# Kernel tuning notes

Hardware: AMD Instinct MI355X
Metric: run time of the kernel (lower is better)

Reference implementation:

```python
import jax, jax.numpy as jnp
import numpy as np

B, N, C = 8, 4096, 512
H = 8
HD = C // H  # 64
SCALE = HD ** -0.5


def setup_inputs() -> dict:
    key = jax.random.key(0)
    ks = jax.random.split(key, 6)
    x = jax.random.normal(ks[0], (B, N, C), dtype=jnp.float32)
    # nn.Linear(dim, dim*3, bias=False): weight [3C, C]
    w_qkv = jax.random.normal(ks[1], (3 * C, C), dtype=jnp.float32) * (C ** -0.5)
    # nn.Linear(dim, dim): weight [C, C], bias [C]
    w_proj = jax.random.normal(ks[2], (C, C), dtype=jnp.float32) * (C ** -0.5)
    b_proj = jnp.zeros((C,), dtype=jnp.float32)
    w_q = jax.random.normal(ks[3], (H, HD), dtype=jnp.float32)
    w_k = jax.random.normal(ks[4], (H, HD), dtype=jnp.float32)
    return {"x": x, "w_qkv": w_qkv, "w_proj": w_proj, "b_proj": b_proj,
            "w_q": w_q, "w_k": w_k}


def reference(x, w_qkv, w_proj, b_proj, w_q, w_k):
    b, n, c = x.shape
    # qkv projection: [B,N,3C] -> (3, B, H, N, HD)
    qkv = jnp.einsum('bnc,dc->bnd', x, w_qkv)
    qkv = qkv.reshape(b, n, 3, H, HD).transpose(2, 0, 3, 1, 4)
    q, k, v = qkv[0], qkv[1], qkv[2]  # each [B,H,N,HD]

    # alpha attention pooling of q -> global query [B,H,HD]
    alpha = jax.nn.softmax(jnp.einsum('bhnc,hc->bhn', q, w_q) * SCALE, axis=-1)
    global_q = jnp.einsum('bhn,bhnc->bhc', alpha, q)

    # p = broadcast global_q over k; beta pooling of k -> global key
    p = global_q[:, :, None, :] * k  # [B,H,N,HD] (attn_drop is identity in eval)
    beta = jax.nn.softmax(jnp.einsum('bhnc,hc->bhn', p, w_k) * SCALE, axis=-1)
    global_k = jnp.einsum('bhn,bhnc->bhc', beta, k)

    # u = global_k broadcast * v, then merge heads
    u = global_k[:, :, None, :] * v  # [B,H,N,HD]
    u_flat = u.transpose(0, 2, 1, 3).reshape(b, n, c)
    q_flat = q.transpose(0, 2, 1, 3).reshape(b, n, c)

    out = jnp.einsum('bnc,dc->bnd', u_flat, w_proj) + b_proj + q_flat
    return out
```

## Files before the change

### kernel.cpp

```cpp
#include <hip/hip_runtime.h>
#include <hip/hip_bf16.h>
#include <math.h>

#define B_  8
#define N_  4096
#define C_  512
#define H_  8
#define HD_ 64
#define M_  (B_*N_)
#define K_  C_
#define D3_ (3*C_)
#define SCALE_ 0.125f
#define CH_ 8
#define CHN (N_/CH_)

using f32x4  = __attribute__((ext_vector_type(4))) float;
using bf16x8 = __attribute__((ext_vector_type(8))) short;

__device__ __forceinline__ unsigned short f2bf(float f) {
    unsigned int u = __builtin_bit_cast(unsigned int, f);
    u += 0x7FFFu + ((u >> 16) & 1u);
    return (unsigned short)(u >> 16);
}
__device__ __forceinline__ float bf2f(unsigned short s) {
    unsigned int u = ((unsigned int)s) << 16;
    return __builtin_bit_cast(float, u);
}

__device__ __forceinline__ void gl_lds16(const void* g, void* l) {
    __builtin_amdgcn_global_load_lds(
        (const __attribute__((address_space(1))) unsigned int*)(g),
        (__attribute__((address_space(3))) unsigned int*)(l), 16, 0, 0);
}

__global__ __launch_bounds__(256, 2)
void k_gemm1(const unsigned short* __restrict__ Ag, const unsigned short* __restrict__ Bg,
             float* __restrict__ outQ, unsigned short* __restrict__ outK,
             unsigned short* __restrict__ outV)
{
    __shared__ __align__(16) unsigned char lds[16384];
    const int m0 = blockIdx.x * 128;
    const int d0 = blockIdx.y * 128;
    const int t = threadIdx.x, lane = t & 63, w = t >> 6;
    const int wr = w >> 1, wc = w & 1;
    const int lrow = lane >> 2, lslot = lane & 3;
    const int fr = lane & 15, g = lane >> 4;

    f32x4 acc[4][4];
    #pragma unroll
    for (int i = 0; i < 4; ++i)
        #pragma unroll
        for (int j = 0; j < 4; ++j) acc[i][j] = (f32x4){0.f,0.f,0.f,0.f};

    for (int k0 = 0; k0 < K_; k0 += 32) {
        #pragma unroll
        for (int s = 0; s < 2; ++s) {
            const int seg = w*2 + s;
            const int row = seg*16 + lrow;
            const int ch  = lslot ^ ((row >> 1) & 3);
            gl_lds16(Ag + (size_t)(m0+row)*K_ + k0 + ch*8, lds + seg*1024);
            gl_lds16(Bg + (size_t)(d0+row)*K_ + k0 + ch*8, lds + 8192 + seg*1024);
        }
        __syncthreads();
        bf16x8 aF[4], bF[4];
        #pragma unroll
        for (int i = 0; i < 4; ++i) {
            const int r = wr*64 + i*16 + fr;
            const int sl = g ^ ((r >> 1) & 3);
            aF[i] = *(const bf16x8*)(lds + r*64 + sl*16);
        }
        #pragma unroll
        for (int j = 0; j < 4; ++j) {
            const int r = wc*64 + j*16 + fr;
            const int sl = g ^ ((r >> 1) & 3);
            bF[j] = *(const bf16x8*)(lds + 8192 + r*64 + sl*16);
        }
        #pragma unroll
        for (int i = 0; i < 4; ++i)
            #pragma unroll
            for (int j = 0; j < 4; ++j)
                acc[i][j] = __builtin_amdgcn_mfma_f32_16x16x32_bf16(aF[i], bF[j], acc[i][j], 0, 0, 0);
        __syncthreads();
    }

    #pragma unroll
    for (int i = 0; i < 4; ++i)
        #pragma unroll
        for (int j = 0; j < 4; ++j) {
            const int trow = wr*64 + i*16 + (lane >> 4)*4;
            const int tcol = wc*64 + j*16 + (lane & 15);
            const int d = d0 + tcol;
            #pragma unroll
            for (int p = 0; p < 4; ++p) {
                const size_t m = (size_t)(m0 + trow + p);
                const float vv = acc[i][j][p];
                if (d0 < C_)          outQ[m*C_ + d] = vv;
                else if (d0 < 2*C_)   outK[m*C_ + (d - C_)] = f2bf(vv);
                else                  outV[m*C_ + (d - 2*C_)] = f2bf(vv);
            }
        }
}

__global__ __launch_bounds__(256, 2)
void k_gemm2(const unsigned short* __restrict__ Ag, const unsigned short* __restrict__ Wpb,
             const float* __restrict__ bproj, float* __restrict__ out)
{
    __shared__ __align__(16) unsigned char lds[16384];
    const int m0 = blockIdx.x * 128;
    const int d0 = blockIdx.y * 128;
    const int b  = m0 >> 12;
    const unsigned short* Bg = Wpb + (size_t)b * C_ * C_;
    const int t = threadIdx.x, lane = t & 63, w = t >> 6;
    const int wr = w >> 1, wc = w & 1;
    const int lrow = lane >> 2, lslot = lane & 3;
    const int fr = lane & 15, g = lane >> 4;

    f32x4 acc[4][4];
    #pragma unroll
    for (int i = 0; i < 4; ++i)
        #pragma unroll
        for (int j = 0; j < 4; ++j) acc[i][j] = (f32x4){0.f,0.f,0.f,0.f};

    for (int k0 = 0; k0 < K_; k0 += 32) {
        #pragma unroll
        for (int s = 0; s < 2; ++s) {
            const int seg = w*2 + s;
            const int row = seg*16 + lrow;
            const int ch  = lslot ^ ((row >> 1) & 3);
            gl_lds16(Ag + (size_t)(m0+row)*K_ + k0 + ch*8, lds + seg*1024);
            gl_lds16(Bg + (size_t)(d0+row)*K_ + k0 + ch*8, lds + 8192 + seg*1024);
        }
        __syncthreads();
        bf16x8 aF[4], bF[4];
        #pragma unroll
        for (int i = 0; i < 4; ++i) {
            const int r = wr*64 + i*16 + fr;
            const int sl = g ^ ((r >> 1) & 3);
            aF[i] = *(const bf16x8*)(lds + r*64 + sl*16);
        }
        #pragma unroll
        for (int j = 0; j < 4; ++j) {
            const int r = wc*64 + j*16 + fr;
            const int sl = g ^ ((r >> 1) & 3);
            bF[j] = *(const bf16x8*)(lds + 8192 + r*64 + sl*16);
        }
        #pragma unroll
        for (int i = 0; i < 4; ++i)
            #pragma unroll
            for (int j = 0; j < 4; ++j)
                acc[i][j] = __builtin_amdgcn_mfma_f32_16x16x32_bf16(aF[i], bF[j], acc[i][j], 0, 0, 0);
        __syncthreads();
    }

    #pragma unroll
    for (int i = 0; i < 4; ++i)
        #pragma unroll
        for (int j = 0; j < 4; ++j) {
            const int trow = wr*64 + i*16 + (lane >> 4)*4;
            const int tcol = wc*64 + j*16 + (lane & 15);
            const int d = d0 + tcol;
            const float bp = bproj[d];
            #pragma unroll
            for (int p = 0; p < 4; ++p) {
                const size_t off = (size_t)(m0 + trow + p)*C_ + d;
                out[off] = acc[i][j][p] + bp + out[off];
            }
        }
}

template<int SRCBF>
__device__ __forceinline__ float loadsrc(const void* s, size_t idx) {
    if constexpr (SRCBF) return bf2f(((const unsigned short*)s)[idx]);
    else                 return ((const float*)s)[idx];
}

template<int SRCBF>
__global__ __launch_bounds__(256)
void k_pool_part(const void* __restrict__ srcv, const float* __restrict__ wvec,
                 const float* __restrict__ gq_in,
                 float* __restrict__ pm, float* __restrict__ ps, float* __restrict__ pv)
{
    __shared__ float sl[CHN];
    __shared__ float red[4];
    __shared__ float stat[2];
    __shared__ float wsum[4][64];
    const int bid = blockIdx.x;
    const int bh = bid >> 3, ch = bid & 7;
    const int b = bh >> 3, h = bh & 7;
    const int t = threadIdx.x, lane = t & 63, wv = t >> 6;

    float w = wvec[h*HD_ + lane];
    if (gq_in) w *= gq_in[bh*HD_ + lane];
    const size_t rowbase = ((size_t)b*N_ + (size_t)ch*CHN)*C_ + h*HD_ + lane;

    for (int n0 = wv*4; n0 < CHN; n0 += 16) {
        float x0 = loadsrc<SRCBF>(srcv, rowbase + (size_t)(n0+0)*C_) * w;
        float x1 = loadsrc<SRCBF>(srcv, rowbase + (size_t)(n0+1)*C_) * w;
        float x2 = loadsrc<SRCBF>(srcv, rowbase + (size_t)(n0+2)*C_) * w;
        float x3 = loadsrc<SRCBF>(srcv, rowbase + (size_t)(n0+3)*C_) * w;
        #pragma unroll
        for (int off = 32; off; off >>= 1) {
            x0 += __shfl_xor(x0, off); x1 += __shfl_xor(x1, off);
            x2 += __shfl_xor(x2, off); x3 += __shfl_xor(x3, off);
        }
        if (lane == 0) {
            sl[n0+0] = x0*SCALE_; sl[n0+1] = x1*SCALE_;
            sl[n0+2] = x2*SCALE_; sl[n0+3] = x3*SCALE_;
        }
    }
    __syncthreads();

    float m = fmaxf(sl[t], sl[t+256]);
    #pragma unroll
    for (int off = 32; off; off >>= 1) m = fmaxf(m, __shfl_xor(m, off));
    if (lane == 0) red[wv] = m;
    __syncthreads();
    if (t == 0) stat[0] = fmaxf(fmaxf(red[0], red[1]), fmaxf(red[2], red[3]));
    __syncthreads();
    m = stat[0];

    float e0 = __expf(sl[t] - m), e1 = __expf(sl[t+256] - m);
    sl[t] = e0; sl[t+256] = e1;
    float s = e0 + e1;
    #pragma unroll
    for (int off = 32; off; off >>= 1) s += __shfl_xor(s, off);
    if (lane == 0) red[wv] = s;
    __syncthreads();
    if (t == 0) stat[1] = red[0] + red[1] + red[2] + red[3];
    __syncthreads();

    float acc = 0.f;
    for (int n0 = wv*4; n0 < CHN; n0 += 16) {
        acc = fmaf(sl[n0+0], loadsrc<SRCBF>(srcv, rowbase + (size_t)(n0+0)*C_), acc);
        acc = fmaf(sl[n0+1], loadsrc<SRCBF>(srcv, rowbase + (size_t)(n0+1)*C_), acc);
        acc = fmaf(sl[n0+2], loadsrc<SRCBF>(srcv, rowbase + (size_t)(n0+2)*C_), acc);
        acc = fmaf(sl[n0+3], loadsrc<SRCBF>(srcv, rowbase + (size_t)(n0+3)*C_), acc);
    }
    wsum[wv][lane] = acc;
    __syncthreads();
    if (t < 64) {
        pv[(size_t)bid*HD_ + t] = wsum[0][t] + wsum[1][t] + wsum[2][t] + wsum[3][t];
        if (t == 0) { pm[bid] = stat[0]; ps[bid] = stat[1]; }
    }
}

__global__ __launch_bounds__(64)
void k_pool_comb(const float* __restrict__ pm, const float* __restrict__ ps,
                 const float* __restrict__ pv, float* __restrict__ gout)
{
    const int bh = blockIdx.x, c = threadIdx.x;
    float m = -1e30f;
    #pragma unroll
    for (int ch = 0; ch < CH_; ++ch) m = fmaxf(m, pm[bh*CH_ + ch]);
    float s = 0.f, g = 0.f;
    #pragma unroll
    for (int ch = 0; ch < CH_; ++ch) {
        const float e = __expf(pm[bh*CH_ + ch] - m);
        s += ps[bh*CH_ + ch] * e;
        g += pv[(size_t)(bh*CH_ + ch)*HD_ + c] * e;
    }
    gout[bh*HD_ + c] = g / s;
}

__global__ void k_cvt(const float* __restrict__ in, unsigned short* __restrict__ o, int n4)
{
    int i = blockIdx.x*blockDim.x + threadIdx.x;
    const int stride = gridDim.x*blockDim.x;
    for (; i < n4; i += stride) {
        const float4 f = ((const float4*)in)[i];
        ushort4 r; r.x = f2bf(f.x); r.y = f2bf(f.y); r.z = f2bf(f.z); r.w = f2bf(f.w);
        ((ushort4*)o)[i] = r;
    }
}

__global__ void k_fold(const float* __restrict__ wp, const float* __restrict__ gkf,
                       unsigned short* __restrict__ wpb)
{
    const int i = blockIdx.x*256 + threadIdx.x;
    const int idx4 = i*4;
    const int b  = idx4 >> 18;
    const int wi = idx4 & 262143;
    const int k  = idx4 & 511;
    const float4 wv4 = *(const float4*)(wp + wi);
    const float* gk = gkf + b*C_ + k;
    ushort4 r;
    r.x = f2bf(wv4.x * gk[0]); r.y = f2bf(wv4.y * gk[1]);
    r.z = f2bf(wv4.z * gk[2]); r.w = f2bf(wv4.w * gk[3]);
    ((ushort4*)wpb)[i] = r;
}

extern "C" void kernel_launch(void* const* d_in, const int* in_sizes, int n_in,
                              void* d_out, int out_size, void* d_ws, size_t ws_size,
                              hipStream_t stream)
{
    (void)in_sizes; (void)n_in; (void)out_size; (void)ws_size;
    const float* x      = (const float*)d_in[0];
    const float* w_qkv  = (const float*)d_in[1];
    const float* w_proj = (const float*)d_in[2];
    const float* b_proj = (const float*)d_in[3];
    const float* w_q    = (const float*)d_in[4];
    const float* w_k    = (const float*)d_in[5];
    float* out = (float*)d_out;

    unsigned short* xb  = (unsigned short*)d_ws;
    unsigned short* wqb = xb  + (size_t)M_*K_;
    unsigned short* kb  = wqb + (size_t)D3_*K_;
    unsigned short* vb  = kb  + (size_t)M_*C_;
    unsigned short* wpb = vb  + (size_t)M_*C_;
    float* gq  = (float*)(wpb + (size_t)8*C_*C_);
    float* gkf = gq  + B_*H_*HD_;
    float* pm  = gkf + B_*H_*HD_;
    float* ps  = pm + 64*CH_;
    float* pv  = ps + 64*CH_;

    k_cvt<<<2048, 256, 0, stream>>>(x, xb, M_*K_/4);
    k_cvt<<<768,  256, 0, stream>>>(w_qkv, wqb, D3_*K_/4);

    dim3 g1(M_/128, D3_/128);
    k_gemm1<<<g1, 256, 0, stream>>>(xb, wqb, out, kb, vb);

    k_pool_part<0><<<64*CH_, 256, 0, stream>>>(out, w_q, nullptr, pm, ps, pv);
    k_pool_comb<<<64, 64, 0, stream>>>(pm, ps, pv, gq);
    k_pool_part<1><<<64*CH_, 256, 0, stream>>>(kb, w_k, gq, pm, ps, pv);
    k_pool_comb<<<64, 64, 0, stream>>>(pm, ps, pv, gkf);

    k_fold<<<2048, 256, 0, stream>>>(w_proj, gkf, wpb);

    dim3 g2(M_/128, C_/128);
    k_gemm2<<<g2, 256, 0, stream>>>(vb, wpb, b_proj, out);
}
```

Before: 308.6 us.

## Fuse alpha pooling into QKV GEMM epilogue and merge pooling stages

The q-side alpha softmax pooling now runs in the GEMM1 epilogue on the accumulators, writing per-16-row partial max/sum/weighted-vector results, so the separate pass that re-reads fp32 q from global memory goes away. The k-side pooling becomes a single-pass online softmax with 16 chunks per head, and the final combine is folded into the weight-fold kernel. The two conversion launches are merged into one. Launch count and memory traffic drop, at the cost of a heavier GEMM1 epilogue with shuffles and exps, plus a larger partial buffer (256 chunks per head) that comb1 must reduce.

```diff
diff --git a/kernel.cpp b/kernel.cpp
--- a/kernel.cpp
+++ b/kernel.cpp
@@ -11,8 +11,6 @@
 #define K_  C_
 #define D3_ (3*C_)
 #define SCALE_ 0.125f
-#define CH_ 8
-#define CHN (N_/CH_)
 
 using f32x4  = __attribute__((ext_vector_type(4))) float;
 using bf16x8 = __attribute__((ext_vector_type(8))) short;
@@ -35,8 +33,10 @@
 
 __global__ __launch_bounds__(256, 2)
 void k_gemm1(const unsigned short* __restrict__ Ag, const unsigned short* __restrict__ Bg,
+             const float* __restrict__ Wq,
              float* __restrict__ outQ, unsigned short* __restrict__ outK,
-             unsigned short* __restrict__ outV)
+             unsigned short* __restrict__ outV,
+             float* __restrict__ pm1, float* __restrict__ ps1, float* __restrict__ pv1)
 {
     __shared__ __align__(16) unsigned char lds[16384];
     const int m0 = blockIdx.x * 128;
@@ -87,8 +87,8 @@
     for (int i = 0; i < 4; ++i)
         #pragma unroll
         for (int j = 0; j < 4; ++j) {
-            const int trow = wr*64 + i*16 + (lane >> 4)*4;
-            const int tcol = wc*64 + j*16 + (lane & 15);
+            const int trow = wr*64 + i*16 + g*4;
+            const int tcol = wc*64 + j*16 + fr;
             const int d = d0 + tcol;
             #pragma unroll
             for (int p = 0; p < 4; ++p) {
@@ -99,6 +99,171 @@
                 else                  outV[m*C_ + (d - 2*C_)] = f2bf(vv);
             }
         }
+
+    if (d0 < C_) {
+        const int head = (d0 >> 6) + wc;
+        const int b = m0 >> 12;
+        const int bh = b*8 + head;
+        const int mchunk = (m0 & 4095) >> 7;
+        const int chunk = mchunk*8 + wr*4 + g;
+        float wqv[4];
+        #pragma unroll
+        for (int j = 0; j < 4; ++j) wqv[j] = Wq[head*HD_ + j*16 + fr] * SCALE_;
+
+        float s[4][4];
+        #pragma unroll
+        for (int i = 0; i < 4; ++i)
+            #pragma unroll
+            for (int p = 0; p < 4; ++p) {
+                float d = acc[i][0][p]*wqv[0] + acc[i][1][p]*wqv[1]
+                        + acc[i][2][p]*wqv[2] + acc[i][3][p]*wqv[3];
+                d += __shfl_xor(d, 1); d += __shfl_xor(d, 2);
+                d += __shfl_xor(d, 4); d += __shfl_xor(d, 8);
+                s[i][p] = d;
+            }
+        float mx = s[0][0];
+        #pragma unroll
+        for (int i = 0; i < 4; ++i)
+            #pragma unroll
+            for (int p = 0; p < 4; ++p) mx = fmaxf(mx, s[i][p]);
+        float e[4][4]; float ssum = 0.f;
+        #pragma unroll
+        for (int i = 0; i < 4; ++i)
+            #pragma unroll
+            for (int p = 0; p < 4; ++p) { e[i][p] = __expf(s[i][p] - mx); ssum += e[i][p]; }
+        #pragma unroll
+        for (int j = 0; j < 4; ++j) {
+            float pvj = 0.f;
+            #pragma unroll
+            for (int i = 0; i < 4; ++i)
+                #pragma unroll
+                for (int p = 0; p < 4; ++p) pvj = fmaf(e[i][p], acc[i][j][p], pvj);
+            pv1[((size_t)bh*256 + chunk)*64 + j*16 + fr] = pvj;
+        }
+        if (fr == 0) { pm1[bh*256 + chunk] = mx; ps1[bh*256 + chunk] = ssum; }
+    }
+}
+
+__global__ __launch_bounds__(256)
+void k_comb1(const float* __restrict__ pm, const float* __restrict__ ps,
+             const float* __restrict__ pv, float* __restrict__ gq)
+{
+    __shared__ float red[4];
+    __shared__ float sred[4];
+    __shared__ float pvs[4][64];
+    __shared__ float stat[2];
+    const int bh = blockIdx.x;
+    const int t = threadIdx.x, lane = t & 63, wv = t >> 6;
+
+    float m = pm[bh*256 + t];
+    #pragma unroll
+    for (int off = 32; off; off >>= 1) m = fmaxf(m, __shfl_xor(m, off));
+    if (lane == 0) red[wv] = m;
+    __syncthreads();
+    if (t == 0) stat[0] = fmaxf(fmaxf(red[0],red[1]), fmaxf(red[2],red[3]));
+    __syncthreads();
+    m = stat[0];
+
+    float e  = __expf(pm[bh*256 + t] - m);
+    float sp = ps[bh*256 + t] * e;
+    #pragma unroll
+    for (int off = 32; off; off >>= 1) sp += __shfl_xor(sp, off);
+    if (lane == 0) sred[wv] = sp;
+    __syncthreads();
+    if (t == 0) stat[1] = sred[0]+sred[1]+sred[2]+sred[3];
+
+    float acc = 0.f;
+    for (int c0 = 0; c0 < 64; ++c0) {
+        const int ch = wv*64 + c0;
+        const float ec = __expf(pm[bh*256 + ch] - m);
+        acc = fmaf(pv[((size_t)bh*256 + ch)*64 + lane], ec, acc);
+    }
+    pvs[wv][lane] = acc;
+    __syncthreads();
+    if (t < 64) gq[bh*64 + t] = (pvs[0][t]+pvs[1][t]+pvs[2][t]+pvs[3][t]) / stat[1];
+}
+
+__global__ __launch_bounds__(256)
+void k_pool2(const unsigned short* __restrict__ kb, const float* __restrict__ w_k,
+             const float* __restrict__ gq,
+             float* __restrict__ pm2, float* __restrict__ ps2, float* __restrict__ pv2)
+{
+    __shared__ float mred[4];
+    __shared__ float sl[4][64];
+    __shared__ float sred2[4];
+    const int bid = blockIdx.x;
+    const int bh = bid >> 4, ch = bid & 15;
+    const int b = bh >> 3, h = bh & 7;
+    const int t = threadIdx.x, lane = t & 63, wv = t >> 6;
+    const float wk = w_k[h*64 + lane] * gq[bh*64 + lane] * SCALE_;
+    const unsigned short* base = kb + ((size_t)b*N_ + ch*256)*C_ + h*64 + lane;
+
+    float mw = -1e30f, sw = 0.f, pvw = 0.f;
+    for (int n0 = wv*4; n0 < 256; n0 += 16) {
+        float x0 = bf2f(base[(size_t)(n0+0)*C_]);
+        float x1 = bf2f(base[(size_t)(n0+1)*C_]);
+        float x2 = bf2f(base[(size_t)(n0+2)*C_]);
+        float x3 = bf2f(base[(size_t)(n0+3)*C_]);
+        float s0 = x0*wk, s1 = x1*wk, s2 = x2*wk, s3 = x3*wk;
+        #pragma unroll
+        for (int off = 32; off; off >>= 1) {
+            s0 += __shfl_xor(s0, off); s1 += __shfl_xor(s1, off);
+            s2 += __shfl_xor(s2, off); s3 += __shfl_xor(s3, off);
+        }
+        const float mx = fmaxf(fmaxf(s0,s1), fmaxf(s2,s3));
+        const float mn = fmaxf(mw, mx);
+        const float f  = __expf(mw - mn);
+        const float e0 = __expf(s0 - mn), e1 = __expf(s1 - mn);
+        const float e2 = __expf(s2 - mn), e3 = __expf(s3 - mn);
+        sw  = sw*f  + (e0+e1+e2+e3);
+        pvw = pvw*f + e0*x0 + e1*x1 + e2*x2 + e3*x3;
+        mw = mn;
+    }
+    if (lane == 0) mred[wv] = mw;
+    __syncthreads();
+    const float mb = fmaxf(fmaxf(mred[0],mred[1]), fmaxf(mred[2],mred[3]));
+    const float f = __expf(mw - mb);
+    sl[wv][lane] = pvw * f;
+    if (lane == 0) sred2[wv] = sw * f;
+    __syncthreads();
+    if (t < 64) {
+        pv2[(size_t)bid*64 + t] = sl[0][t]+sl[1][t]+sl[2][t]+sl[3][t];
+        if (t == 0) ps2[bid] = sred2[0]+sred2[1]+sred2[2]+sred2[3];
+        if (t == 1) pm2[bid] = mb;
+    }
+}
+
+__global__ __launch_bounds__(256)
+void k_fold(const float* __restrict__ wp, const float* __restrict__ pm2,
+            const float* __restrict__ ps2, const float* __restrict__ pv2,
+            unsigned short* __restrict__ wpb)
+{
+    const int i = blockIdx.x*256 + threadIdx.x;
+    const int idx4 = i*4;
+    const int b  = idx4 >> 18;
+    const int wi = idx4 & 262143;
+    const int k  = idx4 & 511;
+    const int h  = k >> 6, hd = k & 63;
+    const int bh = b*8 + h;
+
+    float m = pm2[bh*16];
+    #pragma unroll
+    for (int c = 1; c < 16; ++c) m = fmaxf(m, pm2[bh*16 + c]);
+    float s = 0.f, g0 = 0.f, g1 = 0.f, g2 = 0.f, g3 = 0.f;
+    #pragma unroll
+    for (int c = 0; c < 16; ++c) {
+        const float e = __expf(pm2[bh*16 + c] - m);
+        s = fmaf(ps2[bh*16 + c], e, s);
+        const float4 pvv = *(const float4*)(pv2 + (size_t)(bh*16 + c)*64 + hd);
+        g0 = fmaf(pvv.x, e, g0); g1 = fmaf(pvv.y, e, g1);
+        g2 = fmaf(pvv.z, e, g2); g3 = fmaf(pvv.w, e, g3);
+    }
+    const float inv = 1.0f / s;
+    const float4 wv4 = *(const float4*)(wp + wi);
+    ushort4 r;
+    r.x = f2bf(wv4.x * g0 * inv); r.y = f2bf(wv4.y * g1 * inv);
+    r.z = f2bf(wv4.z * g2 * inv); r.w = f2bf(wv4.w * g3 * inv);
+    ((ushort4*)wpb)[i] = r;
 }
 
 __global__ __launch_bounds__(256, 2)
@@ -156,8 +321,8 @@
     for (int i = 0; i < 4; ++i)
         #pragma unroll
         for (int j = 0; j < 4; ++j) {
-            const int trow = wr*64 + i*16 + (lane >> 4)*4;
-            const int tcol = wc*64 + j*16 + (lane & 15);
+            const int trow = wr*64 + i*16 + g*4;
+            const int tcol = wc*64 + j*16 + fr;
             const int d = d0 + tcol;
             const float bp = bproj[d];
             #pragma unroll
@@ -168,125 +333,25 @@
         }
 }
 
-template<int SRCBF>
-__device__ __forceinline__ float loadsrc(const void* s, size_t idx) {
-    if constexpr (SRCBF) return bf2f(((const unsigned short*)s)[idx]);
-    else                 return ((const float*)s)[idx];
-}
-
-template<int SRCBF>
-__global__ __launch_bounds__(256)
-void k_pool_part(const void* __restrict__ srcv, const float* __restrict__ wvec,
-                 const float* __restrict__ gq_in,
-                 float* __restrict__ pm, float* __restrict__ ps, float* __restrict__ pv)
-{
-    __shared__ float sl[CHN];
-    __shared__ float red[4];
-    __shared__ float stat[2];
-    __shared__ float wsum[4][64];
-    const int bid = blockIdx.x;
-    const int bh = bid >> 3, ch = bid & 7;
-    const int b = bh >> 3, h = bh & 7;
-    const int t = threadIdx.x, lane = t & 63, wv = t >> 6;
-
-    float w = wvec[h*HD_ + lane];
-    if (gq_in) w *= gq_in[bh*HD_ + lane];
-    const size_t rowbase = ((size_t)b*N_ + (size_t)ch*CHN)*C_ + h*HD_ + lane;
-
-    for (int n0 = wv*4; n0 < CHN; n0 += 16) {
-        float x0 = loadsrc<SRCBF>(srcv, rowbase + (size_t)(n0+0)*C_) * w;
-        float x1 = loadsrc<SRCBF>(srcv, rowbase + (size_t)(n0+1)*C_) * w;
-        float x2 = loadsrc<SRCBF>(srcv, rowbase + (size_t)(n0+2)*C_) * w;
-        float x3 = loadsrc<SRCBF>(srcv, rowbase + (size_t)(n0+3)*C_) * w;
-        #pragma unroll
-        for (int off = 32; off; off >>= 1) {
-            x0 += __shfl_xor(x0, off); x1 += __shfl_xor(x1, off);
-            x2 += __shfl_xor(x2, off); x3 += __shfl_xor(x3, off);
-        }
-        if (lane == 0) {
-            sl[n0+0] = x0*SCALE_; sl[n0+1] = x1*SCALE_;
-            sl[n0+2] = x2*SCALE_; sl[n0+3] = x3*SCALE_;
-        }
-    }
-    __syncthreads();
-
-    float m = fmaxf(sl[t], sl[t+256]);
-    #pragma unroll
-    for (int off = 32; off; off >>= 1) m = fmaxf(m, __shfl_xor(m, off));
-    if (lane == 0) red[wv] = m;
-    __syncthreads();
-    if (t == 0) stat[0] = fmaxf(fmaxf(red[0], red[1]), fmaxf(red[2], red[3]));
-    __syncthreads();
-    m = stat[0];
-
-    float e0 = __expf(sl[t] - m), e1 = __expf(sl[t+256] - m);
-    sl[t] = e0; sl[t+256] = e1;
-    float s = e0 + e1;
-    #pragma unroll
-    for (int off = 32; off; off >>= 1) s += __shfl_xor(s, off);
-    if (lane == 0) red[wv] = s;
-    __syncthreads();
-    if (t == 0) stat[1] = red[0] + red[1] + red[2] + red[3];
-    __syncthreads();
-
-    float acc = 0.f;
-    for (int n0 = wv*4; n0 < CHN; n0 += 16) {
-        acc = fmaf(sl[n0+0], loadsrc<SRCBF>(srcv, rowbase + (size_t)(n0+0)*C_), acc);
-        acc = fmaf(sl[n0+1], loadsrc<SRCBF>(srcv, rowbase + (size_t)(n0+1)*C_), acc);
-        acc = fmaf(sl[n0+2], loadsrc<SRCBF>(srcv, rowbase + (size_t)(n0+2)*C_), acc);
-        acc = fmaf(sl[n0+3], loadsrc<SRCBF>(srcv, rowbase + (size_t)(n0+3)*C_), acc);
-    }
-    wsum[wv][lane] = acc;
-    __syncthreads();
-    if (t < 64) {
-        pv[(size_t)bid*HD_ + t] = wsum[0][t] + wsum[1][t] + wsum[2][t] + wsum[3][t];
-        if (t == 0) { pm[bid] = stat[0]; ps[bid] = stat[1]; }
-    }
-}
-
-__global__ __launch_bounds__(64)
-void k_pool_comb(const float* __restrict__ pm, const float* __restrict__ ps,
-                 const float* __restrict__ pv, float* __restrict__ gout)
-{
-    const int bh = blockIdx.x, c = threadIdx.x;
-    float m = -1e30f;
-    #pragma unroll
-    for (int ch = 0; ch < CH_; ++ch) m = fmaxf(m, pm[bh*CH_ + ch]);
-    float s = 0.f, g = 0.f;
-    #pragma unroll
-    for (int ch = 0; ch < CH_; ++ch) {
-        const float e = __expf(pm[bh*CH_ + ch] - m);
-        s += ps[bh*CH_ + ch] * e;
-        g += pv[(size_t)(bh*CH_ + ch)*HD_ + c] * e;
-    }
-    gout[bh*HD_ + c] = g / s;
-}
-
-__global__ void k_cvt(const float* __restrict__ in, unsigned short* __restrict__ o, int n4)
-{
-    int i = blockIdx.x*blockDim.x + threadIdx.x;
-    const int stride = gridDim.x*blockDim.x;
-    for (; i < n4; i += stride) {
-        const float4 f = ((const float4*)in)[i];
-        ushort4 r; r.x = f2bf(f.x); r.y = f2bf(f.y); r.z = f2bf(f.z); r.w = f2bf(f.w);
-        ((ushort4*)o)[i] = r;
-    }
-}
-
-__global__ void k_fold(const float* __restrict__ wp, const float* __restrict__ gkf,
-                       unsigned short* __restrict__ wpb)
-{
-    const int i = blockIdx.x*256 + threadIdx.x;
-    const int idx4 = i*4;
-    const int b  = idx4 >> 18;
-    const int wi = idx4 & 262143;
-    const int k  = idx4 & 511;
-    const float4 wv4 = *(const float4*)(wp + wi);
-    const float* gk = gkf + b*C_ + k;
-    ushort4 r;
-    r.x = f2bf(wv4.x * gk[0]); r.y = f2bf(wv4.y * gk[1]);
-    r.z = f2bf(wv4.z * gk[2]); r.w = f2bf(wv4.w * gk[3]);
-    ((ushort4*)wpb)[i] = r;
+__global__ void k_cvt2(const float* __restrict__ a, const float* __restrict__ bsrc,
+                       unsigned short* __restrict__ oa, unsigned short* __restrict__ ob,
+                       int na4, int nb4)
+{
+    int i = blockIdx.x*256 + threadIdx.x;
+    const int stride = gridDim.x*256;
+    const int tot = na4 + nb4;
+    for (; i < tot; i += stride) {
+        if (i < na4) {
+            const float4 f = ((const float4*)a)[i];
+            ushort4 r; r.x = f2bf(f.x); r.y = f2bf(f.y); r.z = f2bf(f.z); r.w = f2bf(f.w);
+            ((ushort4*)oa)[i] = r;
+        } else {
+            const int j = i - na4;
+            const float4 f = ((const float4*)bsrc)[j];
+            ushort4 r; r.x = f2bf(f.x); r.y = f2bf(f.y); r.z = f2bf(f.z); r.w = f2bf(f.w);
+            ((ushort4*)ob)[j] = r;
+        }
+    }
 }
 
 extern "C" void kernel_launch(void* const* d_in, const int* in_sizes, int n_in,
@@ -308,23 +373,21 @@
     unsigned short* vb  = kb  + (size_t)M_*C_;
     unsigned short* wpb = vb  + (size_t)M_*C_;
     float* gq  = (float*)(wpb + (size_t)8*C_*C_);
-    float* gkf = gq  + B_*H_*HD_;
-    float* pm  = gkf + B_*H_*HD_;
-    float* ps  = pm + 64*CH_;
-    float* pv  = ps + 64*CH_;
-
-    k_cvt<<<2048, 256, 0, stream>>>(x, xb, M_*K_/4);
-    k_cvt<<<768,  256, 0, stream>>>(w_qkv, wqb, D3_*K_/4);
+    float* pm1 = gq  + 64*64;
+    float* ps1 = pm1 + 64*256;
+    float* pv1 = ps1 + 64*256;
+    float* pm2 = pv1 + (size_t)64*256*64;
+    float* ps2 = pm2 + 1024;
+    float* pv2 = ps2 + 1024;
+
+    k_cvt2<<<2048, 256, 0, stream>>>(x, w_qkv, xb, wqb, M_*K_/4, D3_*K_/4);
 
     dim3 g1(M_/128, D3_/128);
-    k_gemm1<<<g1, 256, 0, stream>>>(xb, wqb, out, kb, vb);
-
-    k_pool_part<0><<<64*CH_, 256, 0, stream>>>(out, w_q, nullptr, pm, ps, pv);
-    k_pool_comb<<<64, 64, 0, stream>>>(pm, ps, pv, gq);
-    k_pool_part<1><<<64*CH_, 256, 0, stream>>>(kb, w_k, gq, pm, ps, pv);
-    k_pool_comb<<<64, 64, 0, stream>>>(pm, ps, pv, gkf);
-
-    k_fold<<<2048, 256, 0, stream>>>(w_proj, gkf, wpb);
+    k_gemm1<<<g1, 256, 0, stream>>>(xb, wqb, w_q, out, kb, vb, pm1, ps1, pv1);
+
+    k_comb1<<<64, 256, 0, stream>>>(pm1, ps1, pv1, gq);
+    k_pool2<<<1024, 256, 0, stream>>>(kb, w_k, gq, pm2, ps2, pv2);
+    k_fold<<<2048, 256, 0, stream>>>(w_proj, pm2, ps2, pv2, wpb);
 
     dim3 g2(M_/128, C_/128);
     k_gemm2<<<g2, 256, 0, stream>>>(vb, wpb, b_proj, out);
```

Result: faster. 271.0 us (-12.2%).
